# Optimization experiments

Hardware: AMD Instinct MI355X
Metric: run time of the kernel (lower is better)

## Reference

```python
import jax, jax.numpy as jnp
import numpy as np

DIM = 512
HEADS = 8
HEAD_DIM = DIM // HEADS
MLP = 2048
EPS = 1e-5


def _layer_norm(x, g, b):
    mu = jnp.mean(x, axis=-1, keepdims=True)
    var = jnp.var(x, axis=-1, keepdims=True)
    return (x - mu) * jax.lax.rsqrt(var + EPS) * g + b


def setup_inputs() -> dict:
    key = jax.random.key(0)
    ks = jax.random.split(key, 12)
    s = 1.0 / np.sqrt(DIM)
    sm = 1.0 / np.sqrt(MLP)
    return {
        "x": jax.random.normal(ks[0], (2, 4096, DIM), dtype=jnp.float32),
        "Wq": jax.random.normal(ks[1], (DIM, DIM), dtype=jnp.float32) * s,
        "Wk": jax.random.normal(ks[2], (DIM, DIM), dtype=jnp.float32) * s,
        "Wv": jax.random.normal(ks[3], (DIM, DIM), dtype=jnp.float32) * s,
        "Wo": jax.random.normal(ks[4], (DIM, DIM), dtype=jnp.float32) * s,
        "bo": jnp.zeros((DIM,), dtype=jnp.float32),
        "W1": jax.random.normal(ks[5], (DIM, MLP), dtype=jnp.float32) * s,
        "b1": jnp.zeros((MLP,), dtype=jnp.float32),
        "W2": jax.random.normal(ks[6], (MLP, DIM), dtype=jnp.float32) * sm,
        "b2": jnp.zeros((DIM,), dtype=jnp.float32),
        "g1": jnp.ones((DIM,), dtype=jnp.float32),
        "be1": jnp.zeros((DIM,), dtype=jnp.float32),
        "g2": jnp.ones((DIM,), dtype=jnp.float32),
        "be2": jnp.zeros((DIM,), dtype=jnp.float32),
    }


def reference(x, Wq, Wk, Wv, Wo, bo, W1, b1, W2, b2, g1, be1, g2, be2):
    b, n, d = x.shape
    # --- pre-norm multi-head attention ---
    h = _layer_norm(x, g1, be1)
    q = (h @ Wq).reshape(b, n, HEADS, HEAD_DIM).transpose(0, 2, 1, 3)  # [b,h,n,hd]
    k = (h @ Wk).reshape(b, n, HEADS, HEAD_DIM).transpose(0, 2, 1, 3)
    v = (h @ Wv).reshape(b, n, HEADS, HEAD_DIM).transpose(0, 2, 1, 3)
    scores = jnp.einsum("bhqd,bhkd->bhqk", q, k) / np.sqrt(HEAD_DIM)  # [b,h,n,n]
    attn = jax.nn.softmax(scores, axis=-1)
    out = jnp.einsum("bhqk,bhkd->bhqd", attn, v)
    out = out.transpose(0, 2, 1, 3).reshape(b, n, d)
    x = x + out @ Wo + bo
    # --- pre-norm feed-forward ---
    h2 = _layer_norm(x, g2, be2)
    ff = jax.nn.gelu(h2 @ W1 + b1, approximate=False) @ W2 + b2
    return x + ff
```

## Files before the change

### kernel.cpp

```cpp
#include <hip/hip_runtime.h>
#include <math.h>

#define BB   2
#define SEQ  4096
#define DIM  512
#define NH   8
#define HD   64
#define MLPD 2048
#define ROWS (BB*SEQ)
#define SZ   (ROWS*DIM)
#define EPSV 1e-5f

typedef __attribute__((ext_vector_type(8))) short bf16x8;
typedef __attribute__((ext_vector_type(4))) float f32x4;

#if __has_builtin(__builtin_amdgcn_exp2f)
#define EXP2(x) __builtin_amdgcn_exp2f(x)
#else
#define EXP2(x) exp2f(x)
#endif

__device__ __forceinline__ ushort f2bf(float f) {
    unsigned u = __float_as_uint(f);
    u += 0x7fffu + ((u >> 16) & 1u);
    return (ushort)(u >> 16);
}
__device__ __forceinline__ unsigned pack2bf(float a, float b) {
    return (unsigned)f2bf(a) | ((unsigned)f2bf(b) << 16);
}

__device__ __forceinline__ void gload16(const ushort* g, ushort* l) {
    __builtin_amdgcn_global_load_lds(
        (const __attribute__((address_space(1))) unsigned*)g,
        (__attribute__((address_space(3))) unsigned*)l, 16, 0, 0);
}

__global__ __launch_bounds__(128) void ln_kernel(const float* __restrict__ x,
        const float* __restrict__ g, const float* __restrict__ be,
        ushort* __restrict__ out)
{
    int row = blockIdx.x;
    int tid = threadIdx.x;
    const float4 v = ((const float4*)(x + (size_t)row*DIM))[tid];
    float s  = v.x + v.y + v.z + v.w;
    float ss = v.x*v.x + v.y*v.y + v.z*v.z + v.w*v.w;
    #pragma unroll
    for (int off = 32; off > 0; off >>= 1) {
        s  += __shfl_down(s,  off);
        ss += __shfl_down(ss, off);
    }
    __shared__ float red[4];
    if ((tid & 63) == 0) { red[(tid>>6)*2+0] = s; red[(tid>>6)*2+1] = ss; }
    __syncthreads();
    float sum = red[0] + red[2], sumsq = red[1] + red[3];
    float mu  = sum * (1.0f/DIM);
    float var = sumsq * (1.0f/DIM) - mu*mu;
    float rs  = rsqrtf(var + EPSV);
    float4 gv = ((const float4*)g)[tid];
    float4 bv = ((const float4*)be)[tid];
    ushort4 o;
    o.x = f2bf((v.x - mu)*rs*gv.x + bv.x);
    o.y = f2bf((v.y - mu)*rs*gv.y + bv.y);
    o.z = f2bf((v.z - mu)*rs*gv.z + bv.z);
    o.w = f2bf((v.w - mu)*rs*gv.w + bv.w);
    ((ushort4*)(out + (size_t)row*DIM))[tid] = o;
}

__global__ __launch_bounds__(256) void wtrans_kernel(const float* __restrict__ W,
        ushort* __restrict__ Wt, int K, int N)
{
    __shared__ ushort T[64][65];
    int n0 = blockIdx.x*64, k0 = blockIdx.y*64;
    int tid = threadIdx.x;
    #pragma unroll
    for (int p = 0; p < 4; ++p) {
        int r = p*16 + (tid>>4), c = (tid&15)<<2;
        float4 w4 = *(const float4*)(W + (size_t)(k0+r)*N + n0 + c);
        T[c+0][r] = f2bf(w4.x); T[c+1][r] = f2bf(w4.y);
        T[c+2][r] = f2bf(w4.z); T[c+3][r] = f2bf(w4.w);
    }
    __syncthreads();
    #pragma unroll
    for (int p = 0; p < 4; ++p) {
        int n = p*16 + (tid>>4), k = (tid&15)<<2;
        ushort4 o; o.x = T[n][k]; o.y = T[n][k+1]; o.z = T[n][k+2]; o.w = T[n][k+3];
        *(ushort4*)(Wt + (size_t)(n0+n)*K + k0 + k) = o;
    }
}

__global__ __launch_bounds__(256) void wtrans4_kernel(
        const float* __restrict__ W0, const float* __restrict__ W1,
        const float* __restrict__ W2, const float* __restrict__ W3,
        ushort* __restrict__ Wt)
{
    __shared__ ushort T[64][65];
    int z = blockIdx.z;
    const float* W = (z==0) ? W0 : (z==1) ? W1 : (z==2) ? W2 : W3;
    ushort* Wtz = Wt + (size_t)z*512*512;
    int n0 = blockIdx.x*64, k0 = blockIdx.y*64;
    int tid = threadIdx.x;
    #pragma unroll
    for (int p = 0; p < 4; ++p) {
        int r = p*16 + (tid>>4), c = (tid&15)<<2;
        float4 w4 = *(const float4*)(W + (size_t)(k0+r)*512 + n0 + c);
        T[c+0][r] = f2bf(w4.x); T[c+1][r] = f2bf(w4.y);
        T[c+2][r] = f2bf(w4.z); T[c+3][r] = f2bf(w4.w);
    }
    __syncthreads();
    #pragma unroll
    for (int p = 0; p < 4; ++p) {
        int n = p*16 + (tid>>4), k = (tid&15)<<2;
        ushort4 o; o.x = T[n][k]; o.y = T[n][k+1]; o.z = T[n][k+2]; o.w = T[n][k+3];
        *(ushort4*)(Wtz + (size_t)(n0+n)*512 + k0 + k) = o;
    }
}

template<int BM, int NT>
__global__ __launch_bounds__(NT) void gemm_bf16_kernel(
        const ushort* __restrict__ A,
        const ushort* __restrict__ Wta, const ushort* __restrict__ Wtb, const ushort* __restrict__ Wtc,
        const float* __restrict__ bias, const float* __restrict__ resid,
        void* __restrict__ outv, int M, int Nn, int K, int flags)
{
    constexpr int AISS = (BM*4)/NT;
    constexpr int BISS = 256/NT;
    __shared__ ushort As[2][BM*32];
    __shared__ ushort Bs[2][64*32];
    int tid = threadIdx.x;
    int w = tid >> 6, lane = tid & 63, quad = lane >> 4, col = lane & 15;
    int row0 = blockIdx.y * BM, col0 = blockIdx.x * 64;
    int wm0 = w * 32;

    const ushort* Wt; int wcol0, ostride, obase_col;
    float qscale = 1.0f;
    float* outF = nullptr; ushort* outB = nullptr;
    if (flags & 1) {
        int sel = col0 >> 9;
        Wt = (sel == 0) ? Wta : ((sel == 1) ? Wtb : Wtc);
        wcol0 = col0 & 511; ostride = 512; obase_col = wcol0;
        outB = (ushort*)outv + (size_t)sel * ((size_t)M * 512);
        if (sel == 0) qscale = 0.125f * 1.44269504088896f;
        flags |= 16;
    } else {
        Wt = Wta; wcol0 = col0; ostride = Nn; obase_col = col0;
        if (flags & 16) outB = (ushort*)outv; else outF = (float*)outv;
    }

    f32x4 acc[2][4];
    #pragma unroll
    for (int i = 0; i < 2; ++i)
        #pragma unroll
        for (int j = 0; j < 4; ++j) acc[i][j] = (f32x4){0.f,0.f,0.f,0.f};

    const ushort* Ag = A  + (size_t)(row0  + (tid >> 2))*K + ((tid & 3) << 3);
    const ushort* Bg = Wt + (size_t)(wcol0 + (tid >> 2))*K + ((tid & 3) << 3);

    auto issue = [&](ushort* Ad, ushort* Bd, int ko) {
        #pragma unroll
        for (int it = 0; it < AISS; ++it)
            gload16(Ag + ko + (size_t)(it*(NT/4))*K, Ad + it*NT*8 + tid*8);
        #pragma unroll
        for (int it = 0; it < BISS; ++it)
            gload16(Bg + ko + (size_t)(it*(NT/4))*K, Bd + it*NT*8 + tid*8);
    };
    auto compute = [&](const ushort* Ab, const ushort* Bb) {
        bf16x8 af[2], bfr[4];
        #pragma unroll
        for (int i = 0; i < 2; ++i)
            af[i] = *(const bf16x8*)(Ab + (wm0 + i*16 + col)*32 + quad*8);
        #pragma unroll
        for (int j = 0; j < 4; ++j)
            bfr[j] = *(const bf16x8*)(Bb + (j*16 + col)*32 + quad*8);
        #pragma unroll
        for (int i = 0; i < 2; ++i)
            #pragma unroll
            for (int j = 0; j < 4; ++j)
                acc[i][j] = __builtin_amdgcn_mfma_f32_16x16x32_bf16(af[i], bfr[j], acc[i][j], 0, 0, 0);
    };

    int niter = K >> 5;
    issue(As[0], Bs[0], 0);
    for (int i = 0; i < niter; i += 2) {
        __syncthreads();
        if (i + 1 < niter) issue(As[1], Bs[1], (i+1)*32);
        compute(As[0], Bs[0]);
        __syncthreads();
        if (i + 2 < niter) issue(As[0], Bs[0], (i+2)*32);
        compute(As[1], Bs[1]);
    }

    #pragma unroll
    for (int i = 0; i < 2; ++i) {
        #pragma unroll
        for (int r = 0; r < 4; ++r) {
            int row = row0 + wm0 + i*16 + quad*4 + r;
            #pragma unroll
            for (int j = 0; j < 4; ++j) {
                int oc = obase_col + j*16 + col;
                float o = acc[i][j][r] * qscale;
                if (flags & 8) o += bias[oc];
                if (flags & 2) o = 0.5f*o*(1.f + erff(o*0.70710678118654752f));
                if (flags & 4) o += resid[(size_t)row*ostride + oc];
                if (flags & 16) outB[(size_t)row*ostride + oc] = f2bf(o);
                else            outF[(size_t)row*ostride + oc] = o;
            }
        }
    }
}

__global__ __launch_bounds__(256) void vtrans_kernel(const ushort* __restrict__ v,
                                                     ushort* __restrict__ vt)
{
    int tt = blockIdx.x, bh = blockIdx.y;
    int b = bh >> 3, h = bh & 7;
    int tid = threadIdx.x;
    int d = tid >> 2, t0 = (tid & 3) << 4;
    ushort tmp[16];
    #pragma unroll
    for (int i = 0; i < 16; ++i) {
        int kp = t0 + i;
        int korig = ((kp>>5)*2 + ((kp>>2)&1))*16 + ((kp>>3)&3)*4 + (kp&3);
        tmp[i] = v[(size_t)(b*SEQ + tt*64 + korig)*DIM + h*HD + d];
    }
    unsigned u[8];
    #pragma unroll
    for (int j = 0; j < 8; ++j) u[j] = (unsigned)tmp[2*j] | ((unsigned)tmp[2*j+1] << 16);
    ushort* dst = vt + ((size_t)bh*HD + d)*SEQ + tt*64 + t0;
    *(uint4*)(dst)     = make_uint4(u[0],u[1],u[2],u[3]);
    *(uint4*)(dst + 8) = make_uint4(u[4],u[5],u[6],u[7]);
}

__global__ __launch_bounds__(256) void attn_mfma_kernel(
        const ushort* __restrict__ q, const ushort* __restrict__ k,
        const ushort* __restrict__ vt, ushort* __restrict__ out)
{
    __shared__ ushort Kt[64][72];
    __shared__ ushort Vt[64][72];

    int qt = blockIdx.x, bh = blockIdx.y;
    int b = bh >> 3, h = bh & 7;
    int tid = threadIdx.x;
    int w = tid >> 6, lane = tid & 63;
    int quad = lane >> 4, col = lane & 15;
    int qn0 = qt*128 + w*32;

    bf16x8 aq[2][2];
    #pragma unroll
    for (int mt = 0; mt < 2; ++mt) {
        const ushort* qp = q + (size_t)(b*SEQ + qn0 + mt*16 + col)*DIM + h*HD + quad*8;
        aq[mt][0] = *(const bf16x8*)(qp);
        aq[mt][1] = *(const bf16x8*)(qp + 32);
    }
    const short one_bf = (short)0x3F80;
    const bf16x8 ones = {one_bf,one_bf,one_bf,one_bf,one_bf,one_bf,one_bf,one_bf};

    f32x4 ot[2][4];
    f32x4 ol[2];
    #pragma unroll
    for (int mt = 0; mt < 2; ++mt) {
        ol[mt] = (f32x4){0.f,0.f,0.f,0.f};
        #pragma unroll
        for (int t4 = 0; t4 < 4; ++t4) ot[mt][t4] = (f32x4){0.f,0.f,0.f,0.f};
    }

    int skey = tid >> 2, sd0 = (tid & 3) << 4;

    for (int t = 0; t < SEQ/64; ++t) {
        __syncthreads();
        {
            const ushort* kp = k + (size_t)(b*SEQ + t*64 + skey)*DIM + h*HD + sd0;
            *(bf16x8*)&Kt[skey][sd0]     = *(const bf16x8*)(kp);
            *(bf16x8*)&Kt[skey][sd0 + 8] = *(const bf16x8*)(kp + 8);
            const ushort* vp = vt + ((size_t)bh*HD + skey)*SEQ + t*64 + sd0;
            *(bf16x8*)&Vt[skey][sd0]     = *(const bf16x8*)(vp);
            *(bf16x8*)&Vt[skey][sd0 + 8] = *(const bf16x8*)(vp + 8);
        }
        __syncthreads();

        f32x4 sc[2][4];
        #pragma unroll
        for (int mt = 0; mt < 2; ++mt)
            #pragma unroll
            for (int t4 = 0; t4 < 4; ++t4) sc[mt][t4] = (f32x4){0.f,0.f,0.f,0.f};
        #pragma unroll
        for (int c = 0; c < 2; ++c) {
            bf16x8 kf[4];
            #pragma unroll
            for (int t4 = 0; t4 < 4; ++t4)
                kf[t4] = *(const bf16x8*)&Kt[t4*16 + col][c*32 + quad*8];
            #pragma unroll
            for (int mt = 0; mt < 2; ++mt)
                #pragma unroll
                for (int t4 = 0; t4 < 4; ++t4)
                    sc[mt][t4] = __builtin_amdgcn_mfma_f32_16x16x32_bf16(kf[t4], aq[mt][c], sc[mt][t4], 0, 0, 0);
        }

        union PU { bf16x8 v; uint4 u; };
        PU pb[2][2];
        #pragma unroll
        for (int mt = 0; mt < 2; ++mt)
            #pragma unroll
            for (int c = 0; c < 2; ++c) {
                pb[mt][c].u.x = pack2bf(EXP2(sc[mt][2*c  ][0]), EXP2(sc[mt][2*c  ][1]));
                pb[mt][c].u.y = pack2bf(EXP2(sc[mt][2*c  ][2]), EXP2(sc[mt][2*c  ][3]));
                pb[mt][c].u.z = pack2bf(EXP2(sc[mt][2*c+1][0]), EXP2(sc[mt][2*c+1][1]));
                pb[mt][c].u.w = pack2bf(EXP2(sc[mt][2*c+1][2]), EXP2(sc[mt][2*c+1][3]));
            }

        #pragma unroll
        for (int c = 0; c < 2; ++c) {
            bf16x8 vf[4];
            #pragma unroll
            for (int t4 = 0; t4 < 4; ++t4)
                vf[t4] = *(const bf16x8*)&Vt[t4*16 + col][c*32 + quad*8];
            #pragma unroll
            for (int mt = 0; mt < 2; ++mt) {
                #pragma unroll
                for (int t4 = 0; t4 < 4; ++t4)
                    ot[mt][t4] = __builtin_amdgcn_mfma_f32_16x16x32_bf16(vf[t4], pb[mt][c].v, ot[mt][t4], 0, 0, 0);
                ol[mt] = __builtin_amdgcn_mfma_f32_16x16x32_bf16(ones, pb[mt][c].v, ol[mt], 0, 0, 0);
            }
        }
    }

    #pragma unroll
    for (int mt = 0; mt < 2; ++mt) {
        float inv = 1.0f / ol[mt][0];
        #pragma unroll
        for (int t4 = 0; t4 < 4; ++t4) {
            ushort4 o4;
            o4.x = f2bf(ot[mt][t4][0] * inv);
            o4.y = f2bf(ot[mt][t4][1] * inv);
            o4.z = f2bf(ot[mt][t4][2] * inv);
            o4.w = f2bf(ot[mt][t4][3] * inv);
            *(ushort4*)(out + (size_t)(b*SEQ + qn0 + mt*16 + col)*DIM + h*HD + t4*16 + quad*4) = o4;
        }
    }
}

extern "C" void kernel_launch(void* const* d_in, const int* in_sizes, int n_in,
                              void* d_out, int out_size, void* d_ws, size_t ws_size,
                              hipStream_t stream)
{
    (void)in_sizes; (void)n_in; (void)out_size; (void)ws_size;
    const float* x   = (const float*)d_in[0];
    const float* Wq  = (const float*)d_in[1];
    const float* Wk  = (const float*)d_in[2];
    const float* Wv  = (const float*)d_in[3];
    const float* Wo  = (const float*)d_in[4];
    const float* bo  = (const float*)d_in[5];
    const float* W1  = (const float*)d_in[6];
    const float* b1  = (const float*)d_in[7];
    const float* W2  = (const float*)d_in[8];
    const float* b2  = (const float*)d_in[9];
    const float* g1  = (const float*)d_in[10];
    const float* be1 = (const float*)d_in[11];
    const float* g2  = (const float*)d_in[12];
    const float* be2 = (const float*)d_in[13];

    ushort* u = (ushort*)d_ws;
    float*  x2    = (float*)u;
    ushort* h     = u + 2*(size_t)SZ;
    ushort* qb    = u + 3*(size_t)SZ;
    ushort* kb    = u + 4*(size_t)SZ;
    ushort* vb    = u + 5*(size_t)SZ;
    ushort* vtb   = u + 6*(size_t)SZ;
    ushort* attnb = u + 7*(size_t)SZ;
    ushort* ff1   = u + 3*(size_t)SZ;
    ushort* wqkv  = u + 8*(size_t)SZ;
    ushort* wto   = wqkv + 3*(size_t)512*512;
    ushort* wt1   = wqkv + 4*(size_t)512*512;
    ushort* wt2   = wt1  + (size_t)512*2048;
    float*  outp  = (float*)d_out;

    wtrans4_kernel<<<dim3(8,8,4), 256, 0, stream>>>(Wq, Wk, Wv, Wo, wqkv);
    wtrans_kernel<<<dim3(32,8), 256, 0, stream>>>(W1, wt1, 512, 2048);
    wtrans_kernel<<<dim3(8,32), 256, 0, stream>>>(W2, wt2, 2048, 512);

    ln_kernel<<<ROWS, 128, 0, stream>>>(x, g1, be1, h);
    gemm_bf16_kernel<128,256><<<dim3(1536/64, ROWS/128), 256, 0, stream>>>(
        h, wqkv, wqkv + (size_t)512*512, wqkv + 2*(size_t)512*512,
        nullptr, nullptr, qb, ROWS, 1536, DIM, 1);
    vtrans_kernel<<<dim3(SEQ/64, BB*NH), 256, 0, stream>>>(vb, vtb);
    attn_mfma_kernel<<<dim3(SEQ/128, BB*NH), 256, 0, stream>>>(qb, kb, vtb, attnb);
    gemm_bf16_kernel<64,128><<<dim3(DIM/64, ROWS/64), 128, 0, stream>>>(
        attnb, wto, wto, wto, bo, x, x2, ROWS, DIM, DIM, 8|4);
    ln_kernel<<<ROWS, 128, 0, stream>>>(x2, g2, be2, h);
    gemm_bf16_kernel<128,256><<<dim3(MLPD/64, ROWS/128), 256, 0, stream>>>(
        h, wt1, wt1, wt1, b1, nullptr, ff1, ROWS, MLPD, DIM, 8|2|16);
    gemm_bf16_kernel<64,128><<<dim3(DIM/64, ROWS/64), 128, 0, stream>>>(
        ff1, wt2, wt2, wt2, b2, x2, outp, ROWS, DIM, MLPD, 8|4);
}
```

Baseline: 392.7 us.

## Use 128x128 GEMM tiles for QKV/FF1 and double-buffer attention K/V tiles

Adds a gemm128 kernel in which four waves each compute a 64x64 sub-tile of a 128x128 output tile. It is used for the QKV and first MLP projections to raise MFMA work per LDS load and halve the number of blocks. The attention kernel now double-buffers its K/V tiles in LDS, prefetching the next tile into registers during compute, and drops one barrier per iteration. The cost is more registers per thread (64 accumulators) and more LDS, which may lower occupancy.

```diff
diff --git a/kernel.cpp b/kernel.cpp
--- a/kernel.cpp
+++ b/kernel.cpp
@@ -117,19 +117,96 @@
 
 template<int BM, int NT>
 __global__ __launch_bounds__(NT) void gemm_bf16_kernel(
+        const ushort* __restrict__ A, const ushort* __restrict__ Wt,
+        const float* __restrict__ bias, const float* __restrict__ resid,
+        void* __restrict__ outv, int M, int Nn, int K, int flags)
+{
+    constexpr int AISS = (BM*4)/NT;
+    constexpr int BISS = 256/NT;
+    __shared__ ushort As[2][BM*32];
+    __shared__ ushort Bs[2][64*32];
+    int tid = threadIdx.x;
+    int w = tid >> 6, lane = tid & 63, quad = lane >> 4, col = lane & 15;
+    int row0 = blockIdx.y * BM, col0 = blockIdx.x * 64;
+    int wm0 = w * 32;
+
+    float* outF = nullptr; ushort* outB = nullptr;
+    if (flags & 16) outB = (ushort*)outv; else outF = (float*)outv;
+
+    f32x4 acc[2][4];
+    #pragma unroll
+    for (int i = 0; i < 2; ++i)
+        #pragma unroll
+        for (int j = 0; j < 4; ++j) acc[i][j] = (f32x4){0.f,0.f,0.f,0.f};
+
+    const ushort* Ag = A  + (size_t)(row0 + (tid >> 2))*K + ((tid & 3) << 3);
+    const ushort* Bg = Wt + (size_t)(col0 + (tid >> 2))*K + ((tid & 3) << 3);
+
+    auto issue = [&](ushort* Ad, ushort* Bd, int ko) {
+        #pragma unroll
+        for (int it = 0; it < AISS; ++it)
+            gload16(Ag + ko + (size_t)(it*(NT/4))*K, Ad + it*NT*8 + tid*8);
+        #pragma unroll
+        for (int it = 0; it < BISS; ++it)
+            gload16(Bg + ko + (size_t)(it*(NT/4))*K, Bd + it*NT*8 + tid*8);
+    };
+    auto compute = [&](const ushort* Ab, const ushort* Bb) {
+        bf16x8 af[2], bfr[4];
+        #pragma unroll
+        for (int i = 0; i < 2; ++i)
+            af[i] = *(const bf16x8*)(Ab + (wm0 + i*16 + col)*32 + quad*8);
+        #pragma unroll
+        for (int j = 0; j < 4; ++j)
+            bfr[j] = *(const bf16x8*)(Bb + (j*16 + col)*32 + quad*8);
+        #pragma unroll
+        for (int i = 0; i < 2; ++i)
+            #pragma unroll
+            for (int j = 0; j < 4; ++j)
+                acc[i][j] = __builtin_amdgcn_mfma_f32_16x16x32_bf16(af[i], bfr[j], acc[i][j], 0, 0, 0);
+    };
+
+    int niter = K >> 5;
+    issue(As[0], Bs[0], 0);
+    for (int i = 0; i < niter; i += 2) {
+        __syncthreads();
+        if (i + 1 < niter) issue(As[1], Bs[1], (i+1)*32);
+        compute(As[0], Bs[0]);
+        __syncthreads();
+        if (i + 2 < niter) issue(As[0], Bs[0], (i+2)*32);
+        compute(As[1], Bs[1]);
+    }
+
+    #pragma unroll
+    for (int i = 0; i < 2; ++i) {
+        #pragma unroll
+        for (int r = 0; r < 4; ++r) {
+            int row = row0 + wm0 + i*16 + quad*4 + r;
+            #pragma unroll
+            for (int j = 0; j < 4; ++j) {
+                int oc = col0 + j*16 + col;
+                float o = acc[i][j][r];
+                if (flags & 8) o += bias[oc];
+                if (flags & 2) o = 0.5f*o*(1.f + erff(o*0.70710678118654752f));
+                if (flags & 4) o += resid[(size_t)row*Nn + oc];
+                if (flags & 16) outB[(size_t)row*Nn + oc] = f2bf(o);
+                else            outF[(size_t)row*Nn + oc] = o;
+            }
+        }
+    }
+}
+
+__global__ __launch_bounds__(256) void gemm128_kernel(
         const ushort* __restrict__ A,
         const ushort* __restrict__ Wta, const ushort* __restrict__ Wtb, const ushort* __restrict__ Wtc,
         const float* __restrict__ bias, const float* __restrict__ resid,
         void* __restrict__ outv, int M, int Nn, int K, int flags)
 {
-    constexpr int AISS = (BM*4)/NT;
-    constexpr int BISS = 256/NT;
-    __shared__ ushort As[2][BM*32];
-    __shared__ ushort Bs[2][64*32];
+    __shared__ ushort As[2][128*32];
+    __shared__ ushort Bs[2][128*32];
     int tid = threadIdx.x;
     int w = tid >> 6, lane = tid & 63, quad = lane >> 4, col = lane & 15;
-    int row0 = blockIdx.y * BM, col0 = blockIdx.x * 64;
-    int wm0 = w * 32;
+    int row0 = blockIdx.y * 128, col0 = blockIdx.x * 128;
+    int wm0 = (w >> 1) * 64, wn0 = (w & 1) * 64;
 
     const ushort* Wt; int wcol0, ostride, obase_col;
     float qscale = 1.0f;
@@ -146,33 +223,31 @@
         if (flags & 16) outB = (ushort*)outv; else outF = (float*)outv;
     }
 
-    f32x4 acc[2][4];
-    #pragma unroll
-    for (int i = 0; i < 2; ++i)
+    f32x4 acc[4][4];
+    #pragma unroll
+    for (int i = 0; i < 4; ++i)
         #pragma unroll
         for (int j = 0; j < 4; ++j) acc[i][j] = (f32x4){0.f,0.f,0.f,0.f};
 
     const ushort* Ag = A  + (size_t)(row0  + (tid >> 2))*K + ((tid & 3) << 3);
     const ushort* Bg = Wt + (size_t)(wcol0 + (tid >> 2))*K + ((tid & 3) << 3);
+    size_t i64K = (size_t)64*K;
 
     auto issue = [&](ushort* Ad, ushort* Bd, int ko) {
-        #pragma unroll
-        for (int it = 0; it < AISS; ++it)
-            gload16(Ag + ko + (size_t)(it*(NT/4))*K, Ad + it*NT*8 + tid*8);
-        #pragma unroll
-        for (int it = 0; it < BISS; ++it)
-            gload16(Bg + ko + (size_t)(it*(NT/4))*K, Bd + it*NT*8 + tid*8);
+        gload16(Ag + ko,        Ad + tid*8);
+        gload16(Ag + ko + i64K, Ad + 2048 + tid*8);
+        gload16(Bg + ko,        Bd + tid*8);
+        gload16(Bg + ko + i64K, Bd + 2048 + tid*8);
     };
     auto compute = [&](const ushort* Ab, const ushort* Bb) {
-        bf16x8 af[2], bfr[4];
-        #pragma unroll
-        for (int i = 0; i < 2; ++i)
-            af[i] = *(const bf16x8*)(Ab + (wm0 + i*16 + col)*32 + quad*8);
-        #pragma unroll
-        for (int j = 0; j < 4; ++j)
-            bfr[j] = *(const bf16x8*)(Bb + (j*16 + col)*32 + quad*8);
-        #pragma unroll
-        for (int i = 0; i < 2; ++i)
+        bf16x8 af[4], bfr[4];
+        #pragma unroll
+        for (int i = 0; i < 4; ++i) {
+            af[i]  = *(const bf16x8*)(Ab + (wm0 + i*16 + col)*32 + quad*8);
+            bfr[i] = *(const bf16x8*)(Bb + (wn0 + i*16 + col)*32 + quad*8);
+        }
+        #pragma unroll
+        for (int i = 0; i < 4; ++i)
             #pragma unroll
             for (int j = 0; j < 4; ++j)
                 acc[i][j] = __builtin_amdgcn_mfma_f32_16x16x32_bf16(af[i], bfr[j], acc[i][j], 0, 0, 0);
@@ -190,13 +265,13 @@
     }
 
     #pragma unroll
-    for (int i = 0; i < 2; ++i) {
+    for (int i = 0; i < 4; ++i) {
         #pragma unroll
         for (int r = 0; r < 4; ++r) {
             int row = row0 + wm0 + i*16 + quad*4 + r;
             #pragma unroll
             for (int j = 0; j < 4; ++j) {
-                int oc = obase_col + j*16 + col;
+                int oc = obase_col + wn0 + j*16 + col;
                 float o = acc[i][j][r] * qscale;
                 if (flags & 8) o += bias[oc];
                 if (flags & 2) o = 0.5f*o*(1.f + erff(o*0.70710678118654752f));
@@ -234,8 +309,8 @@
         const ushort* __restrict__ q, const ushort* __restrict__ k,
         const ushort* __restrict__ vt, ushort* __restrict__ out)
 {
-    __shared__ ushort Kt[64][72];
-    __shared__ ushort Vt[64][72];
+    __shared__ ushort Kt[2][64][72];
+    __shared__ ushort Vt[2][64][72];
 
     int qt = blockIdx.x, bh = blockIdx.y;
     int b = bh >> 3, h = bh & 7;
@@ -264,18 +339,29 @@
     }
 
     int skey = tid >> 2, sd0 = (tid & 3) << 4;
+    bf16x8 kr[2], vr[2];
+    auto load_tile = [&](int t) {
+        const ushort* kp = k + (size_t)(b*SEQ + t*64 + skey)*DIM + h*HD + sd0;
+        kr[0] = *(const bf16x8*)(kp);
+        kr[1] = *(const bf16x8*)(kp + 8);
+        const ushort* vp = vt + ((size_t)bh*HD + skey)*SEQ + t*64 + sd0;
+        vr[0] = *(const bf16x8*)(vp);
+        vr[1] = *(const bf16x8*)(vp + 8);
+    };
+    auto store_tile = [&](int p) {
+        *(bf16x8*)&Kt[p][skey][sd0]     = kr[0];
+        *(bf16x8*)&Kt[p][skey][sd0+8]   = kr[1];
+        *(bf16x8*)&Vt[p][skey][sd0]     = vr[0];
+        *(bf16x8*)&Vt[p][skey][sd0+8]   = vr[1];
+    };
+
+    load_tile(0);
+    store_tile(0);
+    __syncthreads();
 
     for (int t = 0; t < SEQ/64; ++t) {
-        __syncthreads();
-        {
-            const ushort* kp = k + (size_t)(b*SEQ + t*64 + skey)*DIM + h*HD + sd0;
-            *(bf16x8*)&Kt[skey][sd0]     = *(const bf16x8*)(kp);
-            *(bf16x8*)&Kt[skey][sd0 + 8] = *(const bf16x8*)(kp + 8);
-            const ushort* vp = vt + ((size_t)bh*HD + skey)*SEQ + t*64 + sd0;
-            *(bf16x8*)&Vt[skey][sd0]     = *(const bf16x8*)(vp);
-            *(bf16x8*)&Vt[skey][sd0 + 8] = *(const bf16x8*)(vp + 8);
-        }
-        __syncthreads();
+        int p = t & 1;
+        if (t + 1 < SEQ/64) load_tile(t + 1);
 
         f32x4 sc[2][4];
         #pragma unroll
@@ -287,7 +373,7 @@
             bf16x8 kf[4];
             #pragma unroll
             for (int t4 = 0; t4 < 4; ++t4)
-                kf[t4] = *(const bf16x8*)&Kt[t4*16 + col][c*32 + quad*8];
+                kf[t4] = *(const bf16x8*)&Kt[p][t4*16 + col][c*32 + quad*8];
             #pragma unroll
             for (int mt = 0; mt < 2; ++mt)
                 #pragma unroll
@@ -312,7 +398,7 @@
             bf16x8 vf[4];
             #pragma unroll
             for (int t4 = 0; t4 < 4; ++t4)
-                vf[t4] = *(const bf16x8*)&Vt[t4*16 + col][c*32 + quad*8];
+                vf[t4] = *(const bf16x8*)&Vt[p][t4*16 + col][c*32 + quad*8];
             #pragma unroll
             for (int mt = 0; mt < 2; ++mt) {
                 #pragma unroll
@@ -321,6 +407,9 @@
                 ol[mt] = __builtin_amdgcn_mfma_f32_16x16x32_bf16(ones, pb[mt][c].v, ol[mt], 0, 0, 0);
             }
         }
+
+        if (t + 1 < SEQ/64) store_tile(p ^ 1);
+        __syncthreads();
     }
 
     #pragma unroll
@@ -378,16 +467,16 @@
     wtrans_kernel<<<dim3(8,32), 256, 0, stream>>>(W2, wt2, 2048, 512);
 
     ln_kernel<<<ROWS, 128, 0, stream>>>(x, g1, be1, h);
-    gemm_bf16_kernel<128,256><<<dim3(1536/64, ROWS/128), 256, 0, stream>>>(
+    gemm128_kernel<<<dim3(1536/128, ROWS/128), 256, 0, stream>>>(
         h, wqkv, wqkv + (size_t)512*512, wqkv + 2*(size_t)512*512,
         nullptr, nullptr, qb, ROWS, 1536, DIM, 1);
     vtrans_kernel<<<dim3(SEQ/64, BB*NH), 256, 0, stream>>>(vb, vtb);
     attn_mfma_kernel<<<dim3(SEQ/128, BB*NH), 256, 0, stream>>>(qb, kb, vtb, attnb);
     gemm_bf16_kernel<64,128><<<dim3(DIM/64, ROWS/64), 128, 0, stream>>>(
-        attnb, wto, wto, wto, bo, x, x2, ROWS, DIM, DIM, 8|4);
+        attnb, wto, bo, x, x2, ROWS, DIM, DIM, 8|4);
     ln_kernel<<<ROWS, 128, 0, stream>>>(x2, g2, be2, h);
-    gemm_bf16_kernel<128,256><<<dim3(MLPD/64, ROWS/128), 256, 0, stream>>>(
+    gemm128_kernel<<<dim3(MLPD/128, ROWS/128), 256, 0, stream>>>(
         h, wt1, wt1, wt1, b1, nullptr, ff1, ROWS, MLPD, DIM, 8|2|16);
     gemm_bf16_kernel<64,128><<<dim3(DIM/64, ROWS/64), 128, 0, stream>>>(
-        ff1, wt2, wt2, wt2, b2, x2, outp, ROWS, DIM, MLPD, 8|4);
-}
+        ff1, wt2, b2, x2, outp, ROWS, DIM, MLPD, 8|4);
+}
```

Result: no change. 388.8 us (-1.0%).

## Double-buffer K/V tiles in attention and truncate P to bf16

Applied to the files above, without the earlier changes.

The attention kernel now keeps two LDS buffers for K and V tiles. It prefetches the next tile into registers while computing on the current one and writes it to the other buffer after the MFMAs, so each iteration needs one barrier instead of two. Separately, softmax probabilities are packed to bf16 by truncation instead of round-to-nearest, which saves ALU work but adds a small bias to P. The prefetch costs extra registers and doubles LDS use, which may lower occupancy.

```diff
diff --git a/kernel.cpp b/kernel.cpp
--- a/kernel.cpp
+++ b/kernel.cpp
@@ -27,6 +27,9 @@
 }
 __device__ __forceinline__ unsigned pack2bf(float a, float b) {
     return (unsigned)f2bf(a) | ((unsigned)f2bf(b) << 16);
+}
+__device__ __forceinline__ unsigned pack2bf_tr(float a, float b) {
+    return (__float_as_uint(a) >> 16) | (__float_as_uint(b) & 0xffff0000u);
 }
 
 __device__ __forceinline__ void gload16(const ushort* g, ushort* l) {
@@ -234,8 +237,8 @@
         const ushort* __restrict__ q, const ushort* __restrict__ k,
         const ushort* __restrict__ vt, ushort* __restrict__ out)
 {
-    __shared__ ushort Kt[64][72];
-    __shared__ ushort Vt[64][72];
+    __shared__ ushort Kt[2][64][72];
+    __shared__ ushort Vt[2][64][72];
 
     int qt = blockIdx.x, bh = blockIdx.y;
     int b = bh >> 3, h = bh & 7;
@@ -264,18 +267,29 @@
     }
 
     int skey = tid >> 2, sd0 = (tid & 3) << 4;
+    bf16x8 kr[2], vr[2];
+    auto load_tile = [&](int t) {
+        const ushort* kp = k + (size_t)(b*SEQ + t*64 + skey)*DIM + h*HD + sd0;
+        kr[0] = *(const bf16x8*)(kp);
+        kr[1] = *(const bf16x8*)(kp + 8);
+        const ushort* vp = vt + ((size_t)bh*HD + skey)*SEQ + t*64 + sd0;
+        vr[0] = *(const bf16x8*)(vp);
+        vr[1] = *(const bf16x8*)(vp + 8);
+    };
+    auto store_tile = [&](int p) {
+        *(bf16x8*)&Kt[p][skey][sd0]     = kr[0];
+        *(bf16x8*)&Kt[p][skey][sd0+8]   = kr[1];
+        *(bf16x8*)&Vt[p][skey][sd0]     = vr[0];
+        *(bf16x8*)&Vt[p][skey][sd0+8]   = vr[1];
+    };
+
+    load_tile(0);
+    store_tile(0);
+    __syncthreads();
 
     for (int t = 0; t < SEQ/64; ++t) {
-        __syncthreads();
-        {
-            const ushort* kp = k + (size_t)(b*SEQ + t*64 + skey)*DIM + h*HD + sd0;
-            *(bf16x8*)&Kt[skey][sd0]     = *(const bf16x8*)(kp);
-            *(bf16x8*)&Kt[skey][sd0 + 8] = *(const bf16x8*)(kp + 8);
-            const ushort* vp = vt + ((size_t)bh*HD + skey)*SEQ + t*64 + sd0;
-            *(bf16x8*)&Vt[skey][sd0]     = *(const bf16x8*)(vp);
-            *(bf16x8*)&Vt[skey][sd0 + 8] = *(const bf16x8*)(vp + 8);
-        }
-        __syncthreads();
+        int p = t & 1;
+        if (t + 1 < SEQ/64) load_tile(t + 1);
 
         f32x4 sc[2][4];
         #pragma unroll
@@ -287,7 +301,7 @@
             bf16x8 kf[4];
             #pragma unroll
             for (int t4 = 0; t4 < 4; ++t4)
-                kf[t4] = *(const bf16x8*)&Kt[t4*16 + col][c*32 + quad*8];
+                kf[t4] = *(const bf16x8*)&Kt[p][t4*16 + col][c*32 + quad*8];
             #pragma unroll
             for (int mt = 0; mt < 2; ++mt)
                 #pragma unroll
@@ -301,10 +315,10 @@
         for (int mt = 0; mt < 2; ++mt)
             #pragma unroll
             for (int c = 0; c < 2; ++c) {
-                pb[mt][c].u.x = pack2bf(EXP2(sc[mt][2*c  ][0]), EXP2(sc[mt][2*c  ][1]));
-                pb[mt][c].u.y = pack2bf(EXP2(sc[mt][2*c  ][2]), EXP2(sc[mt][2*c  ][3]));
-                pb[mt][c].u.z = pack2bf(EXP2(sc[mt][2*c+1][0]), EXP2(sc[mt][2*c+1][1]));
-                pb[mt][c].u.w = pack2bf(EXP2(sc[mt][2*c+1][2]), EXP2(sc[mt][2*c+1][3]));
+                pb[mt][c].u.x = pack2bf_tr(EXP2(sc[mt][2*c  ][0]), EXP2(sc[mt][2*c  ][1]));
+                pb[mt][c].u.y = pack2bf_tr(EXP2(sc[mt][2*c  ][2]), EXP2(sc[mt][2*c  ][3]));
+                pb[mt][c].u.z = pack2bf_tr(EXP2(sc[mt][2*c+1][0]), EXP2(sc[mt][2*c+1][1]));
+                pb[mt][c].u.w = pack2bf_tr(EXP2(sc[mt][2*c+1][2]), EXP2(sc[mt][2*c+1][3]));
             }
 
         #pragma unroll
@@ -312,7 +326,7 @@
             bf16x8 vf[4];
             #pragma unroll
             for (int t4 = 0; t4 < 4; ++t4)
-                vf[t4] = *(const bf16x8*)&Vt[t4*16 + col][c*32 + quad*8];
+                vf[t4] = *(const bf16x8*)&Vt[p][t4*16 + col][c*32 + quad*8];
             #pragma unroll
             for (int mt = 0; mt < 2; ++mt) {
                 #pragma unroll
@@ -321,6 +335,9 @@
                 ol[mt] = __builtin_amdgcn_mfma_f32_16x16x32_bf16(ones, pb[mt][c].v, ol[mt], 0, 0, 0);
             }
         }
+
+        if (t + 1 < SEQ/64) store_tile(p ^ 1);
+        __syncthreads();
     }
 
     #pragma unroll
```

Measured after the change: 364.3 us. -7.2%, faster.
